# Performance work log

Measured on AMD Instinct MI355X. Metric: run time of the kernel, lower is better.

The kernel has to match this reference:

```python
import jax, jax.numpy as jnp
import numpy as np

T, B, D, H = 512, 256, 256, 256


def setup_inputs() -> dict:
    key = jax.random.key(0)
    ks = jax.random.split(key, 8)
    x = jax.random.normal(ks[0], (T, B, D), dtype=jnp.float32)
    h0 = jax.random.normal(ks[1], (1, B, H), dtype=jnp.float32)
    c0 = jax.random.normal(ks[2], (1, B, H), dtype=jnp.float32)
    W_ih = jax.random.normal(ks[3], (4 * H, D), dtype=jnp.float32) / np.sqrt(D)
    W_hh = jax.random.normal(ks[4], (4 * H, H), dtype=jnp.float32) / np.sqrt(H)
    b_ih = jnp.zeros((4 * H,), dtype=jnp.float32)
    b_hh = jnp.zeros((4 * H,), dtype=jnp.float32)
    done = jax.random.randint(ks[5], (T, B), 0, 2, dtype=jnp.int32)
    return {"x": x, "h0": h0, "c0": c0, "W_ih": W_ih, "W_hh": W_hh,
            "b_ih": b_ih, "b_hh": b_hh, "done": done}


def reference(x, h0, c0, W_ih, W_hh, b_ih, b_hh, done):
    done_f = done.astype(x.dtype)  # [T, B]
    # Precompute input contribution to gates for all timesteps: [T, B, 4H]
    gx = jnp.einsum('tbd,gd->tbg', x, W_ih) + b_ih + b_hh

    def step(carry, inp):
        h, c = carry                      # [B, H] each
        gxt, dt = inp                     # [B, 4H], [B]
        mask = (1.0 - dt)[:, None]        # reset hidden state where done
        h = h * mask
        c = c * mask
        gates = gxt + jnp.einsum('bh,gh->bg', h, W_hh)  # [B, 4H]
        i, f, g, o = jnp.split(gates, 4, axis=-1)       # PyTorch LSTM gate order
        c = jax.nn.sigmoid(f) * c + jax.nn.sigmoid(i) * jnp.tanh(g)
        h = jax.nn.sigmoid(o) * jnp.tanh(c)
        return (h, c), h

    (hT, cT), feats = jax.lax.scan(step, (h0[0], c0[0]), (gx, done_f))
    rnn_feature = feats.reshape(T * B, H)
    return rnn_feature, hT[None], cT[None]
```

## Files before the change

kernel.cpp:

```cpp
#include <hip/hip_runtime.h>
#include <math.h>

#define T_DIM 512
#define B_DIM 256
#define D_DIM 256
#define H_DIM 256
#define G_DIM 1024
#define K_DIM 512
#define NROUNDS 40
#define CHAIN_K 16

typedef __attribute__((ext_vector_type(8))) short short8;
typedef __attribute__((ext_vector_type(4))) float f32x4;

__device__ __forceinline__ unsigned int f2bf(float f) {
    unsigned int b = __float_as_uint(f);
    return (b + 0x7FFFu + ((b >> 16) & 1u)) >> 16;
}
__device__ __forceinline__ unsigned long long pack4(float4 v) {
    const unsigned int lo = (f2bf(v.y) << 16) | f2bf(v.x);
    const unsigned int hi = (f2bf(v.w) << 16) | f2bf(v.z);
    return ((unsigned long long)hi << 32) | lo;
}
__device__ __forceinline__ float sigm(float x) { return 1.0f / (1.0f + __expf(-x)); }
__device__ __forceinline__ float tanh_fast(float x) { return 2.0f / (1.0f + __expf(-2.0f * x)) - 1.0f; }

__device__ __forceinline__ void dma16(const void* g, void* l) {
    __builtin_amdgcn_global_load_lds(
        (const __attribute__((address_space(1))) void*)g,
        (__attribute__((address_space(3))) void*)l, 16, 0, 0);
}

__global__ __launch_bounds__(256) void k_prep_weights(
    const float* __restrict__ W_ih, const float* __restrict__ W_hh,
    const float* __restrict__ b_ih, const float* __restrict__ b_hh,
    unsigned int* __restrict__ Wb, float* __restrict__ bias)
{
    const int idx = blockIdx.x * 256 + threadIdx.x;
    const int jp = idx & 3, l = (idx >> 2) & 63, ks = (idx >> 8) & 15, nt = idx >> 12;
    const int g = nt * 16 + (l & 15);
    const int k0 = ks * 32 + ((l >> 4) << 3) + 2 * jp;
    const float w0 = (k0 < D_DIM) ? W_ih[g * D_DIM + k0] : W_hh[g * H_DIM + (k0 - D_DIM)];
    const float w1 = (k0 + 1 < D_DIM) ? W_ih[g * D_DIM + k0 + 1] : W_hh[g * H_DIM + (k0 + 1 - D_DIM)];
    Wb[idx] = (f2bf(w1) << 16) | f2bf(w0);
    if (idx < G_DIM) bias[idx] = b_ih[idx] + b_hh[idx];
}

__global__ __launch_bounds__(256) void k_prep_wq(
    const float* __restrict__ W_ih, const float* __restrict__ W_hh,
    unsigned long long* __restrict__ Wq)
{
    const int idx = blockIdx.x * 256 + threadIdx.x;
    const int kq = idx >> 10, g = idx & (G_DIM - 1);
    float w[4];
    #pragma unroll
    for (int j = 0; j < 4; ++j) {
        const int k = kq * 4 + j;
        w[j] = (k < D_DIM) ? W_ih[g * D_DIM + k] : W_hh[g * H_DIM + (k - D_DIM)];
    }
    Wq[idx] = pack4((float4){w[0], w[1], w[2], w[3]});
}

__global__ __launch_bounds__(256) void k_prep_ab(
    const float* __restrict__ x, const float* __restrict__ h0,
    const int* __restrict__ done, unsigned long long* __restrict__ ab_u64)
{
    const int pos = (blockIdx.x * 256 + threadIdx.x) >> 6;
    const int l = threadIdx.x & 63;
    const float4 xv = *(const float4*)(x + (size_t)pos * D_DIM + l * 4);
    ab_u64[(size_t)pos * 128 + l] = pack4(xv);
    const int d = done[pos];
    if (d || pos < B_DIM) {
        unsigned long long hv = 0ull;
        if (!d) {
            const float4 h = *(const float4*)(h0 + (size_t)(pos & (B_DIM - 1)) * H_DIM + l * 4);
            hv = pack4(h);
        }
        ab_u64[(size_t)pos * 128 + 64 + l] = hv;
    }
}

__global__ __launch_bounds__(256) void k_kmap(
    const int* __restrict__ done, int* __restrict__ kmap, int* __restrict__ counts)
{
    __shared__ int lcnt[NROUNDS];
    const int tid = threadIdx.x;
    if (tid < NROUNDS) lcnt[tid] = 0;
    __syncthreads();
    const int t = blockIdx.x, b = tid;
    int kv = t;
    for (int tt = t; tt >= 0; --tt) {
        if (done[tt * B_DIM + b]) { kv = t - tt; break; }
    }
    kmap[t * B_DIM + b] = kv;
    const int bin = kv < NROUNDS ? kv : NROUNDS - 1;
    atomicAdd(&lcnt[bin], 1);
    __syncthreads();
    if (tid < NROUNDS && lcnt[tid] > 0) atomicAdd(&counts[tid], lcnt[tid]);
}

__global__ __launch_bounds__(64) void k_offs(
    const int* __restrict__ counts, int* __restrict__ offs, int* __restrict__ cursor)
{
    if (threadIdx.x == 0) {
        int s = 0;
        for (int i = 0; i < NROUNDS; ++i) { offs[i] = s; s += counts[i]; }
    }
    if (threadIdx.x < NROUNDS) cursor[threadIdx.x] = 0;
}

__global__ __launch_bounds__(256) void k_scatter(
    const int* __restrict__ kmap, const int* __restrict__ offs,
    int* __restrict__ cursor, int* __restrict__ rowlist)
{
    __shared__ int lcnt[NROUNDS];
    __shared__ int gbase[NROUNDS];
    const int tid = threadIdx.x;
    if (tid < NROUNDS) lcnt[tid] = 0;
    __syncthreads();
    const int pos = blockIdx.x * 256 + tid;
    const int kv0 = kmap[pos];
    const int kv = kv0 < NROUNDS ? kv0 : NROUNDS - 1;
    const int lrank = atomicAdd(&lcnt[kv], 1);
    __syncthreads();
    if (tid < NROUNDS && lcnt[tid] > 0) gbase[tid] = atomicAdd(&cursor[tid], lcnt[tid]);
    __syncthreads();
    rowlist[offs[kv] + gbase[kv] + lrank] = pos;
}

__global__ __launch_bounds__(512, 1) void k_round(
    const short* __restrict__ ab, const float* __restrict__ c0,
    const int* __restrict__ done,
    const short* __restrict__ Wb, const float* __restrict__ bias,
    const int* __restrict__ counts, const int* __restrict__ offs,
    const int* __restrict__ rowlist,
    float* __restrict__ out, float* __restrict__ c_buf,
    short* __restrict__ ab_w, int kk)
{
    __shared__ short A_lds[2 * 32 * 512];
    __shared__ float scr[4 * 64 * 36];
    const int nk = counts[kk];
    const int base = offs[kk];
    const int ntiles = (nk + 31) >> 5;

    int cb, rt, rstride;
    if (gridDim.x == 256) {
        const int xcd = blockIdx.x & 7, slot = blockIdx.x >> 3;
        cb = slot & 3;
        rt = xcd * 8 + (slot >> 2);
        rstride = 64;
    } else {
        cb = blockIdx.x & 3;
        rt = blockIdx.x >> 2;
        rstride = gridDim.x >> 2;
    }
    if (rt >= ntiles) return;

    const int tid = threadIdx.x;
    const int w = tid >> 6, l = tid & 63;
    const int lr = l >> 4, lc = l & 15;
    const int q = w & 3, gth = w >> 2;

    const int u_ep = cb * 64 + l;
    const float bI = bias[u_ep], bF = bias[256 + u_ep], bG = bias[512 + u_ep], bO = bias[768 + u_ep];

#define ISSUE_A(PP, bufv)                                                        \
    {                                                                            \
        _Pragma("unroll") for (int rr = 0; rr < 4; ++rr) {                       \
            const int r_ = w * 4 + rr;                                           \
            dma16(ab + (size_t)PP[rr] * 512 + ((l ^ (r_ & 15)) << 3),            \
                  &A_lds[(bufv) * 16384 + r_ * 512]);                            \
        }                                                                        \
    }
#define LOAD_NEXT(row0v, PP, CP, DN, DS)                                         \
    {                                                                            \
        _Pragma("unroll") for (int j_ = 0; j_ < 4; ++j_) {                       \
            const int gr_ = (row0v) + w * 4 + j_;                                \
            PP[j_] = rowlist[base + (gr_ < nk ? gr_ : nk - 1)];                  \
        }                                                                        \
        _Pragma("unroll") for (int j_ = 0; j_ < 4; ++j_) {                       \
            const int p_ = PP[j_];                                               \
            if (kk > 0) {                                                        \
                CP[j_] = c_buf[(size_t)(p_ - B_DIM) * H_DIM + u_ep];             \
                DN[j_] = 0;                                                      \
            } else {                                                             \
                DN[j_] = done[p_];                                               \
                CP[j_] = c0[(size_t)(p_ & (B_DIM - 1)) * H_DIM + u_ep];          \
            }                                                                    \
            const int sp_ = p_ + B_DIM;                                          \
            DS[j_] = (sp_ < T_DIM * B_DIM) ? done[sp_] : 1;                      \
        }                                                                        \
    }

    int posC[4], dnC[4], dsC[4]; float cpC[4];
    LOAD_NEXT(rt * 32, posC, cpC, dnC, dsC);
    ISSUE_A(posC, 0);
    short8 breg0[16], breg1[16];
    {
        const int nt0 = (2 * gth + 0) * 16 + cb * 4 + q;
        const int nt1 = (2 * gth + 1) * 16 + cb * 4 + q;
        #pragma unroll
        for (int ks = 0; ks < 16; ++ks) {
            breg0[ks] = *(const short8*)(Wb + (((size_t)nt0 * 16 + ks) * 64 + l) * 8);
            breg1[ks] = *(const short8*)(Wb + (((size_t)nt1 * 16 + ks) * 64 + l) * 8);
        }
        #pragma unroll
        for (int ks = 0; ks < 16; ++ks) {
            asm volatile("" : "+v"(breg0[ks]));
            asm volatile("" : "+v"(breg1[ks]));
        }
    }

    int buf = 0;
    for (; rt < ntiles; rt += rstride) {
        const int row0 = rt * 32;

        asm volatile("s_waitcnt vmcnt(0) lgkmcnt(0)" ::: "memory");
        __builtin_amdgcn_sched_barrier(0);
        __builtin_amdgcn_s_barrier();
        __builtin_amdgcn_sched_barrier(0);
        const int rtn = rt + rstride;
        const bool more = (rtn < ntiles);
        int posN[4], dnN[4], dsN[4]; float cpN[4];
        if (more) {
            LOAD_NEXT(rtn * 32, posN, cpN, dnN, dsN);
            ISSUE_A(posN, buf ^ 1);
        }

        f32x4 acc0[2], acc1[2];
        #pragma unroll
        for (int mb = 0; mb < 2; ++mb) { acc0[mb] = (f32x4){0,0,0,0}; acc1[mb] = (f32x4){0,0,0,0}; }
        #pragma unroll
        for (int ks = 0; ks < 16; ++ks) {
            #pragma unroll
            for (int mb = 0; mb < 2; ++mb) {
                const short8 a = *(const short8*)&A_lds[buf * 16384 + (mb * 16 + lc) * 512
                                                       + (((ks * 4 + lr) ^ lc) << 3)];
                acc0[mb] = __builtin_amdgcn_mfma_f32_16x16x32_bf16(a, breg0[ks], acc0[mb], 0, 0, 0);
                acc1[mb] = __builtin_amdgcn_mfma_f32_16x16x32_bf16(a, breg1[ks], acc1[mb], 0, 0, 0);
            }
        }

        #pragma unroll
        for (int mb = 0; mb < 2; ++mb) {
            *(f32x4*)&scr[(((2 * gth + 0) * 64 + q * 16 + lc) * 36) + mb * 16 + lr * 4] = acc0[mb];
            *(f32x4*)&scr[(((2 * gth + 1) * 64 + q * 16 + lc) * 36) + mb * 16 + lr * 4] = acc1[mb];
        }
        asm volatile("s_waitcnt lgkmcnt(0)" ::: "memory");
        __builtin_amdgcn_sched_barrier(0);
        __builtin_amdgcn_s_barrier();
        __builtin_amdgcn_sched_barrier(0);

        const f32x4 vi = *(const f32x4*)&scr[((0 * 64 + l) * 36) + w * 4];
        const f32x4 vf = *(const f32x4*)&scr[((1 * 64 + l) * 36) + w * 4];
        const f32x4 vg = *(const f32x4*)&scr[((2 * 64 + l) * 36) + w * 4];
        const f32x4 vo = *(const f32x4*)&scr[((3 * 64 + l) * 36) + w * 4];
        #pragma unroll
        for (int j = 0; j < 4; ++j) {
            const int gr = row0 + w * 4 + j;
            if (gr < nk) {
                const int pos = posC[j];
                const float cp = dnC[j] ? 0.0f : cpC[j];
                const float si = sigm(vi[j] + bI);
                const float sf = sigm(vf[j] + bF);
                const float tg = tanh_fast(vg[j] + bG);
                const float so = sigm(vo[j] + bO);
                const float cn = sf * cp + si * tg;
                const float hn = so * tanh_fast(cn);
                c_buf[(size_t)pos * H_DIM + u_ep] = cn;
                out[(size_t)pos * H_DIM + u_ep]  = hn;
                if (kk + 1 < CHAIN_K && !dsC[j]) {
                    ab_w[(size_t)(pos + B_DIM) * 512 + 256 + u_ep] = (short)f2bf(hn);
                }
            }
        }

        #pragma unroll
        for (int j = 0; j < 4; ++j) { posC[j] = posN[j]; cpC[j] = cpN[j]; dnC[j] = dnN[j]; dsC[j] = dsN[j]; }
        buf ^= 1;
    }
#undef ISSUE_A
#undef LOAD_NEXT
}

__global__ __launch_bounds__(1024) void k_finish(
    const float* __restrict__ x, const unsigned long long* __restrict__ Wq,
    const float* __restrict__ bias,
    const int* __restrict__ counts, const int* __restrict__ offs,
    const int* __restrict__ rowlist, const int* __restrict__ kmap,
    float* __restrict__ out, float* __restrict__ c_buf)
{
    __shared__ float abuf[K_DIM];
    __shared__ float dots[G_DIM];
    const int g = threadIdx.x;
    const int nch = counts[CHAIN_K];

    for (int m = blockIdx.x; m < nch; m += gridDim.x) {
        const int pos0 = rowlist[offs[CHAIN_K] + m];
        float c_u = 0.0f;
        if (g < H_DIM) {
            abuf[H_DIM + g] = out[(size_t)(pos0 - B_DIM) * H_DIM + g];
            c_u = c_buf[(size_t)(pos0 - B_DIM) * H_DIM + g];
        }
        int pos = pos0, step = CHAIN_K;
        while (true) {
            if (g < H_DIM) abuf[g] = x[(size_t)pos * D_DIM + g];
            __syncthreads();
            float dot = bias[g];
            #pragma unroll 8
            for (int kq = 0; kq < K_DIM / 4; ++kq) {
                const unsigned long long wq = Wq[(size_t)kq * G_DIM + g];
                const float4 a = *(const float4*)&abuf[kq * 4];
                const unsigned int wlo = (unsigned int)wq;
                const unsigned int whi = (unsigned int)(wq >> 32);
                const float w0 = __uint_as_float(wlo << 16);
                const float w1 = __uint_as_float(wlo & 0xFFFF0000u);
                const float w2 = __uint_as_float(whi << 16);
                const float w3 = __uint_as_float(whi & 0xFFFF0000u);
                dot = fmaf(a.x, w0, dot);
                dot = fmaf(a.y, w1, dot);
                dot = fmaf(a.z, w2, dot);
                dot = fmaf(a.w, w3, dot);
            }
            dots[g] = dot;
            __syncthreads();
            if (g < H_DIM) {
                const float si = sigm(dots[g]);
                const float sf = sigm(dots[H_DIM + g]);
                const float tg = tanh_fast(dots[2 * H_DIM + g]);
                const float so = sigm(dots[3 * H_DIM + g]);
                c_u = sf * c_u + si * tg;
                const float hn = so * tanh_fast(c_u);
                out[(size_t)pos * H_DIM + g]   = hn;
                c_buf[(size_t)pos * H_DIM + g] = c_u;
                abuf[H_DIM + g] = hn;
            }
            pos += B_DIM;
            ++step;
            __syncthreads();
            if (pos >= T_DIM * B_DIM) break;
            if (kmap[pos] != step) break;
        }
        __syncthreads();
    }
}

__global__ __launch_bounds__(256) void k_final(const float* __restrict__ c_buf, float* __restrict__ out)
{
    const size_t i = (size_t)blockIdx.x * 256 + threadIdx.x;
    const size_t featN = (size_t)T_DIM * B_DIM * H_DIM;
    const size_t last  = (size_t)(T_DIM - 1) * B_DIM * H_DIM;
    out[featN + i] = out[last + i];
    out[featN + (size_t)B_DIM * H_DIM + i] = c_buf[last + i];
}

__global__ __launch_bounds__(64) void k_zero(int* __restrict__ counts)
{
    if (threadIdx.x < NROUNDS) counts[threadIdx.x] = 0;
}

extern "C" void kernel_launch(void* const* d_in, const int* in_sizes, int n_in,
                              void* d_out, int out_size, void* d_ws, size_t ws_size,
                              hipStream_t stream)
{
    const float* x    = (const float*)d_in[0];
    const float* h0   = (const float*)d_in[1];
    const float* c0   = (const float*)d_in[2];
    const float* W_ih = (const float*)d_in[3];
    const float* W_hh = (const float*)d_in[4];
    const float* b_ih = (const float*)d_in[5];
    const float* b_hh = (const float*)d_in[6];
    const int*   done = (const int*)d_in[7];
    float* out = (float*)d_out;

    const size_t TB = (size_t)T_DIM * B_DIM;
    char* ws = (char*)d_ws;
    size_t off = 0;
    float* c_buf = (float*)(ws + off);            off += TB * H_DIM * 4;
    unsigned int* Wb = (unsigned int*)(ws + off); off += (size_t)(K_DIM / 2) * G_DIM * 4;
    unsigned long long* Wq = (unsigned long long*)(ws + off); off += (size_t)(K_DIM / 4) * G_DIM * 8;
    float* bias = (float*)(ws + off);             off += (size_t)G_DIM * 4;
    int* kmap    = (int*)(ws + off);              off += TB * 4;
    int* rowlist = (int*)(ws + off);              off += TB * 4;
    int* counts  = (int*)(ws + off);              off += 256;
    int* offs    = (int*)(ws + off);              off += 256;
    int* cursor  = (int*)(ws + off);              off += 256;
    off = (off + 255) & ~(size_t)255;
    short* ab = (short*)(ws + off);               off += TB * 512 * 2;

    k_zero<<<1, 64, 0, stream>>>(counts);
    k_prep_weights<<<1024, 256, 0, stream>>>(W_ih, W_hh, b_ih, b_hh, Wb, bias);
    k_prep_wq<<<512, 256, 0, stream>>>(W_ih, W_hh, Wq);
    k_prep_ab<<<(int)(TB / 4), 256, 0, stream>>>(x, h0, done, (unsigned long long*)ab);
    k_kmap<<<T_DIM, 256, 0, stream>>>(done, kmap, counts);
    k_offs<<<1, 64, 0, stream>>>(counts, offs, cursor);
    k_scatter<<<(int)(TB / 256), 256, 0, stream>>>(kmap, offs, cursor, rowlist);

    int est = 70000;
    for (int k = 0; k < CHAIN_K; ++k) {
        int rgs = (est + 31) / 32;
        if (rgs > 64) rgs = 64;
        if (rgs < 1) rgs = 1;
        k_round<<<4 * rgs, 512, 0, stream>>>((const short*)ab, c0, done, (const short*)Wb,
                                             bias, counts, offs, rowlist, out, c_buf, ab, k);
        est >>= 1;
    }
    k_finish<<<64, 1024, 0, stream>>>(x, Wq, bias, counts, offs, rowlist, kmap, out, c_buf);
    k_final<<<B_DIM * H_DIM / 256, 256, 0, stream>>>(c_buf, out);
}
```

Baseline: 550.6 us.

## Fuse chained LSTM round kernels into one persistent cooperative kernel with grid sync

```diff
diff --git a/kernel.cpp b/kernel.cpp
--- a/kernel.cpp
+++ b/kernel.cpp
@@ -1,5 +1,8 @@
 #include <hip/hip_runtime.h>
+#include <hip/hip_cooperative_groups.h>
 #include <math.h>
+
+namespace cg = cooperative_groups;
 
 #define T_DIM 512
 #define B_DIM 256
@@ -128,41 +131,88 @@
     rowlist[offs[kv] + gbase[kv] + lrank] = pos;
 }
 
-__global__ __launch_bounds__(512, 1) void k_round(
-    const short* __restrict__ ab, const float* __restrict__ c0,
-    const int* __restrict__ done,
-    const short* __restrict__ Wb, const float* __restrict__ bias,
-    const int* __restrict__ counts, const int* __restrict__ offs,
-    const int* __restrict__ rowlist,
-    float* __restrict__ out, float* __restrict__ c_buf,
-    short* __restrict__ ab_w, int kk)
-{
-    __shared__ short A_lds[2 * 32 * 512];
-    __shared__ float scr[4 * 64 * 36];
-    const int nk = counts[kk];
-    const int base = offs[kk];
-    const int ntiles = (nk + 31) >> 5;
-
-    int cb, rt, rstride;
-    if (gridDim.x == 256) {
-        const int xcd = blockIdx.x & 7, slot = blockIdx.x >> 3;
-        cb = slot & 3;
-        rt = xcd * 8 + (slot >> 2);
-        rstride = 64;
-    } else {
-        cb = blockIdx.x & 3;
-        rt = blockIdx.x >> 2;
-        rstride = gridDim.x >> 2;
-    }
-    if (rt >= ntiles) return;
-
-    const int tid = threadIdx.x;
-    const int w = tid >> 6, l = tid & 63;
-    const int lr = l >> 4, lc = l & 15;
-    const int q = w & 3, gth = w >> 2;
-
-    const int u_ep = cb * 64 + l;
-    const float bI = bias[u_ep], bF = bias[256 + u_ep], bG = bias[512 + u_ep], bO = bias[768 + u_ep];
+#define ROUND_BODY(AB, C0, DONE, COUNTS, OFFS, ROWLIST, OUT, CBUF, ABW, KK)       \
+    {                                                                             \
+        const int nk = COUNTS[KK];                                                \
+        const int base = OFFS[KK];                                                \
+        const int ntiles = (nk + 31) >> 5;                                        \
+        int rt = rt0;                                                             \
+        if (rt < ntiles) {                                                        \
+            int posC[4], dnC[4], dsC[4]; float cpC[4];                            \
+            LOAD_NEXT(rt * 32, posC, cpC, dnC, dsC, KK);                          \
+            ISSUE_A(posC, 0);                                                     \
+            int buf = 0;                                                          \
+            for (; rt < ntiles; rt += rstride) {                                  \
+                const int row0 = rt * 32;                                         \
+                asm volatile("s_waitcnt vmcnt(0) lgkmcnt(0)" ::: "memory");       \
+                __builtin_amdgcn_sched_barrier(0);                                \
+                __builtin_amdgcn_s_barrier();                                     \
+                __builtin_amdgcn_sched_barrier(0);                                \
+                const int rtn = rt + rstride;                                     \
+                const bool more = (rtn < ntiles);                                 \
+                int posN[4], dnN[4], dsN[4]; float cpN[4];                        \
+                if (more) {                                                       \
+                    LOAD_NEXT(rtn * 32, posN, cpN, dnN, dsN, KK);                 \
+                    ISSUE_A(posN, buf ^ 1);                                       \
+                }                                                                 \
+                f32x4 acc0[2], acc1[2];                                           \
+                acc0[0] = (f32x4){0,0,0,0}; acc0[1] = (f32x4){0,0,0,0};           \
+                acc1[0] = (f32x4){0,0,0,0}; acc1[1] = (f32x4){0,0,0,0};           \
+                _Pragma("unroll")                                                 \
+                for (int ks = 0; ks < 16; ++ks) {                                 \
+                    _Pragma("unroll")                                             \
+                    for (int mb = 0; mb < 2; ++mb) {                              \
+                        const short8 a = *(const short8*)&A_lds[buf * 16384       \
+                            + (mb * 16 + lc) * 512 + (((ks * 4 + lr) ^ lc) << 3)];\
+                        acc0[mb] = __builtin_amdgcn_mfma_f32_16x16x32_bf16(       \
+                            a, breg0[ks], acc0[mb], 0, 0, 0);                     \
+                        acc1[mb] = __builtin_amdgcn_mfma_f32_16x16x32_bf16(       \
+                            a, breg1[ks], acc1[mb], 0, 0, 0);                     \
+                    }                                                             \
+                }                                                                 \
+                _Pragma("unroll")                                                 \
+                for (int mb = 0; mb < 2; ++mb) {                                  \
+                    *(f32x4*)&scr[(((2 * gth + 0) * 64 + q * 16 + lc) * 36)       \
+                                  + mb * 16 + lr * 4] = acc0[mb];                 \
+                    *(f32x4*)&scr[(((2 * gth + 1) * 64 + q * 16 + lc) * 36)       \
+                                  + mb * 16 + lr * 4] = acc1[mb];                 \
+                }                                                                 \
+                asm volatile("s_waitcnt lgkmcnt(0)" ::: "memory");                \
+                __builtin_amdgcn_sched_barrier(0);                                \
+                __builtin_amdgcn_s_barrier();                                     \
+                __builtin_amdgcn_sched_barrier(0);                                \
+                const f32x4 vi = *(const f32x4*)&scr[((0 * 64 + l) * 36) + w * 4];\
+                const f32x4 vf = *(const f32x4*)&scr[((1 * 64 + l) * 36) + w * 4];\
+                const f32x4 vg = *(const f32x4*)&scr[((2 * 64 + l) * 36) + w * 4];\
+                const f32x4 vo = *(const f32x4*)&scr[((3 * 64 + l) * 36) + w * 4];\
+                _Pragma("unroll")                                                 \
+                for (int j = 0; j < 4; ++j) {                                     \
+                    const int gr = row0 + w * 4 + j;                              \
+                    if (gr < nk) {                                                \
+                        const int pos = posC[j];                                  \
+                        const float cp = dnC[j] ? 0.0f : cpC[j];                  \
+                        const float si = sigm(vi[j] + bI);                        \
+                        const float sf = sigm(vf[j] + bF);                        \
+                        const float tg = tanh_fast(vg[j] + bG);                   \
+                        const float so = sigm(vo[j] + bO);                        \
+                        const float cn = sf * cp + si * tg;                       \
+                        const float hn = so * tanh_fast(cn);                      \
+                        CBUF[(size_t)pos * H_DIM + u_ep] = cn;                    \
+                        OUT[(size_t)pos * H_DIM + u_ep]  = hn;                    \
+                        if (KK + 1 < CHAIN_K && !dsC[j])                          \
+                            ABW[(size_t)(pos + B_DIM) * 512 + 256 + u_ep]         \
+                                = (short)f2bf(hn);                                \
+                    }                                                             \
+                }                                                                 \
+                _Pragma("unroll")                                                 \
+                for (int j = 0; j < 4; ++j) {                                     \
+                    posC[j] = posN[j]; cpC[j] = cpN[j];                           \
+                    dnC[j] = dnN[j]; dsC[j] = dsN[j];                             \
+                }                                                                 \
+                buf ^= 1;                                                         \
+            }                                                                     \
+        }                                                                         \
+    }
 
 #define ISSUE_A(PP, bufv)                                                        \
     {                                                                            \
@@ -172,15 +222,16 @@
                   &A_lds[(bufv) * 16384 + r_ * 512]);                            \
         }                                                                        \
     }
-#define LOAD_NEXT(row0v, PP, CP, DN, DS)                                         \
+#define LOAD_NEXT(row0v, PP, CP, DN, DS, KK)                                     \
     {                                                                            \
+        const int nkl = counts[KK]; const int basel = offs[KK];                  \
         _Pragma("unroll") for (int j_ = 0; j_ < 4; ++j_) {                       \
             const int gr_ = (row0v) + w * 4 + j_;                                \
-            PP[j_] = rowlist[base + (gr_ < nk ? gr_ : nk - 1)];                  \
+            PP[j_] = rowlist[basel + (gr_ < nkl ? gr_ : nkl - 1)];               \
         }                                                                        \
         _Pragma("unroll") for (int j_ = 0; j_ < 4; ++j_) {                       \
             const int p_ = PP[j_];                                               \
-            if (kk > 0) {                                                        \
+            if (KK > 0) {                                                        \
                 CP[j_] = c_buf[(size_t)(p_ - B_DIM) * H_DIM + u_ep];             \
                 DN[j_] = 0;                                                      \
             } else {                                                             \
@@ -192,9 +243,30 @@
         }                                                                        \
     }
 
-    int posC[4], dnC[4], dsC[4]; float cpC[4];
-    LOAD_NEXT(rt * 32, posC, cpC, dnC, dsC);
-    ISSUE_A(posC, 0);
+__global__ __launch_bounds__(512, 1) void k_rounds_coop(
+    const short* __restrict__ ab, const float* __restrict__ c0,
+    const int* __restrict__ done,
+    const short* __restrict__ Wb, const float* __restrict__ bias,
+    const int* __restrict__ counts, const int* __restrict__ offs,
+    const int* __restrict__ rowlist,
+    float* __restrict__ out, float* __restrict__ c_buf,
+    short* __restrict__ ab_w)
+{
+    cg::grid_group grid = cg::this_grid();
+    __shared__ short A_lds[2 * 32 * 512];
+    __shared__ float scr[4 * 64 * 36];
+
+    const int tid = threadIdx.x;
+    const int w = tid >> 6, l = tid & 63;
+    const int lr = l >> 4, lc = l & 15;
+    const int q = w & 3, gth = w >> 2;
+    const int xcd = blockIdx.x & 7, slot = blockIdx.x >> 3;
+    const int cb = slot & 3;
+    const int rt0 = xcd * 8 + (slot >> 2);
+    const int rstride = 64;
+    const int u_ep = cb * 64 + l;
+    const float bI = bias[u_ep], bF = bias[256 + u_ep], bG = bias[512 + u_ep], bO = bias[768 + u_ep];
+
     short8 breg0[16], breg1[16];
     {
         const int nt0 = (2 * gth + 0) * 16 + cb * 4 + q;
@@ -211,76 +283,62 @@
         }
     }
 
-    int buf = 0;
-    for (; rt < ntiles; rt += rstride) {
-        const int row0 = rt * 32;
-
-        asm volatile("s_waitcnt vmcnt(0) lgkmcnt(0)" ::: "memory");
-        __builtin_amdgcn_sched_barrier(0);
-        __builtin_amdgcn_s_barrier();
-        __builtin_amdgcn_sched_barrier(0);
-        const int rtn = rt + rstride;
-        const bool more = (rtn < ntiles);
-        int posN[4], dnN[4], dsN[4]; float cpN[4];
-        if (more) {
-            LOAD_NEXT(rtn * 32, posN, cpN, dnN, dsN);
-            ISSUE_A(posN, buf ^ 1);
-        }
-
-        f32x4 acc0[2], acc1[2];
-        #pragma unroll
-        for (int mb = 0; mb < 2; ++mb) { acc0[mb] = (f32x4){0,0,0,0}; acc1[mb] = (f32x4){0,0,0,0}; }
+    #pragma unroll 1
+    for (int kk = 0; kk < CHAIN_K; ++kk) {
+        ROUND_BODY(ab, c0, done, counts, offs, rowlist, out, c_buf, ab_w, kk);
+        __threadfence();
+        grid.sync();
+        __threadfence();
+    }
+}
+
+__global__ __launch_bounds__(512, 1) void k_round(
+    const short* __restrict__ ab, const float* __restrict__ c0,
+    const int* __restrict__ done,
+    const short* __restrict__ Wb, const float* __restrict__ bias,
+    const int* __restrict__ counts, const int* __restrict__ offs,
+    const int* __restrict__ rowlist,
+    float* __restrict__ out, float* __restrict__ c_buf,
+    short* __restrict__ ab_w, int kk)
+{
+    __shared__ short A_lds[2 * 32 * 512];
+    __shared__ float scr[4 * 64 * 36];
+    const int tid = threadIdx.x;
+    const int w = tid >> 6, l = tid & 63;
+    const int lr = l >> 4, lc = l & 15;
+    const int q = w & 3, gth = w >> 2;
+
+    int cb, rt0, rstride;
+    if (gridDim.x == 256) {
+        const int xcd = blockIdx.x & 7, slot = blockIdx.x >> 3;
+        cb = slot & 3;
+        rt0 = xcd * 8 + (slot >> 2);
+        rstride = 64;
+    } else {
+        cb = blockIdx.x & 3;
+        rt0 = blockIdx.x >> 2;
+        rstride = gridDim.x >> 2;
+    }
+    const int u_ep = cb * 64 + l;
+    const float bI = bias[u_ep], bF = bias[256 + u_ep], bG = bias[512 + u_ep], bO = bias[768 + u_ep];
+
+    short8 breg0[16], breg1[16];
+    {
+        const int nt0 = (2 * gth + 0) * 16 + cb * 4 + q;
+        const int nt1 = (2 * gth + 1) * 16 + cb * 4 + q;
         #pragma unroll
         for (int ks = 0; ks < 16; ++ks) {
-            #pragma unroll
-            for (int mb = 0; mb < 2; ++mb) {
-                const short8 a = *(const short8*)&A_lds[buf * 16384 + (mb * 16 + lc) * 512
-                                                       + (((ks * 4 + lr) ^ lc) << 3)];
-                acc0[mb] = __builtin_amdgcn_mfma_f32_16x16x32_bf16(a, breg0[ks], acc0[mb], 0, 0, 0);
-                acc1[mb] = __builtin_amdgcn_mfma_f32_16x16x32_bf16(a, breg1[ks], acc1[mb], 0, 0, 0);
-            }
-        }
-
+            breg0[ks] = *(const short8*)(Wb + (((size_t)nt0 * 16 + ks) * 64 + l) * 8);
+            breg1[ks] = *(const short8*)(Wb + (((size_t)nt1 * 16 + ks) * 64 + l) * 8);
+        }
         #pragma unroll
-        for (int mb = 0; mb < 2; ++mb) {
-            *(f32x4*)&scr[(((2 * gth + 0) * 64 + q * 16 + lc) * 36) + mb * 16 + lr * 4] = acc0[mb];
-            *(f32x4*)&scr[(((2 * gth + 1) * 64 + q * 16 + lc) * 36) + mb * 16 + lr * 4] = acc1[mb];
-        }
-        asm volatile("s_waitcnt lgkmcnt(0)" ::: "memory");
-        __builtin_amdgcn_sched_barrier(0);
-        __builtin_amdgcn_s_barrier();
-        __builtin_amdgcn_sched_barrier(0);
-
-        const f32x4 vi = *(const f32x4*)&scr[((0 * 64 + l) * 36) + w * 4];
-        const f32x4 vf = *(const f32x4*)&scr[((1 * 64 + l) * 36) + w * 4];
-        const f32x4 vg = *(const f32x4*)&scr[((2 * 64 + l) * 36) + w * 4];
-        const f32x4 vo = *(const f32x4*)&scr[((3 * 64 + l) * 36) + w * 4];
-        #pragma unroll
-        for (int j = 0; j < 4; ++j) {
-            const int gr = row0 + w * 4 + j;
-            if (gr < nk) {
-                const int pos = posC[j];
-                const float cp = dnC[j] ? 0.0f : cpC[j];
-                const float si = sigm(vi[j] + bI);
-                const float sf = sigm(vf[j] + bF);
-                const float tg = tanh_fast(vg[j] + bG);
-                const float so = sigm(vo[j] + bO);
-                const float cn = sf * cp + si * tg;
-                const float hn = so * tanh_fast(cn);
-                c_buf[(size_t)pos * H_DIM + u_ep] = cn;
-                out[(size_t)pos * H_DIM + u_ep]  = hn;
-                if (kk + 1 < CHAIN_K && !dsC[j]) {
-                    ab_w[(size_t)(pos + B_DIM) * 512 + 256 + u_ep] = (short)f2bf(hn);
-                }
-            }
-        }
-
-        #pragma unroll
-        for (int j = 0; j < 4; ++j) { posC[j] = posN[j]; cpC[j] = cpN[j]; dnC[j] = dnN[j]; dsC[j] = dsN[j]; }
-        buf ^= 1;
-    }
-#undef ISSUE_A
-#undef LOAD_NEXT
+        for (int ks = 0; ks < 16; ++ks) {
+            asm volatile("" : "+v"(breg0[ks]));
+            asm volatile("" : "+v"(breg1[ks]));
+        }
+    }
+
+    ROUND_BODY(ab, c0, done, counts, offs, rowlist, out, c_buf, ab_w, kk);
 }
 
 __global__ __launch_bounds__(1024) void k_finish(
@@ -396,14 +454,23 @@
     k_offs<<<1, 64, 0, stream>>>(counts, offs, cursor);
     k_scatter<<<(int)(TB / 256), 256, 0, stream>>>(kmap, offs, cursor, rowlist);
 
-    int est = 70000;
-    for (int k = 0; k < CHAIN_K; ++k) {
-        int rgs = (est + 31) / 32;
-        if (rgs > 64) rgs = 64;
-        if (rgs < 1) rgs = 1;
-        k_round<<<4 * rgs, 512, 0, stream>>>((const short*)ab, c0, done, (const short*)Wb,
-                                             bias, counts, offs, rowlist, out, c_buf, ab, k);
-        est >>= 1;
+    const short* ab_c = (const short*)ab;
+    const short* Wb_s = (const short*)Wb;
+    void* args[] = {(void*)&ab_c, (void*)&c0, (void*)&done, (void*)&Wb_s, (void*)&bias,
+                    (void*)&counts, (void*)&offs, (void*)&rowlist,
+                    (void*)&out, (void*)&c_buf, (void*)&ab};
+    hipError_t ce = hipLaunchCooperativeKernel((void*)k_rounds_coop,
+                                               dim3(256), dim3(512), args, 0, stream);
+    if (ce != hipSuccess) {
+        int est = 70000;
+        for (int k = 0; k < CHAIN_K; ++k) {
+            int rgs = (est + 31) / 32;
+            if (rgs > 64) rgs = 64;
+            if (rgs < 1) rgs = 1;
+            k_round<<<4 * rgs, 512, 0, stream>>>(ab_c, c0, done, Wb_s, bias,
+                                                 counts, offs, rowlist, out, c_buf, ab, k);
+            est >>= 1;
+        }
     }
     k_finish<<<64, 1024, 0, stream>>>(x, Wq, bias, counts, offs, rowlist, kmap, out, c_buf);
     k_final<<<B_DIM * H_DIM / 256, 256, 0, stream>>>(c_buf, out);
```

After: 2.002 ms. 264% more time.
